# Kernel optimization log

Hardware: AMD Instinct MI355X
Metric: run time of the kernel (lower is better)

Reference implementation:

```python
import jax, jax.numpy as jnp
import numpy as np

NEG_SLOPE = 0.2


def add_self_loops(edge_index, num_nodes):
    loop = jnp.arange(num_nodes, dtype=edge_index.dtype)
    return jnp.concatenate([edge_index, jnp.stack([loop, loop])], axis=1)


def gat_conv(x, edge_index, W, att_src, att_dst, bias, heads, out_ch, concat):
    # x: [N, F_in]; edge_index: [2, E]; W: [F_in, heads*out_ch]
    # att_src/att_dst: [heads, out_ch]; bias: [heads*out_ch] or [out_ch]
    N = x.shape[0]
    ei = add_self_loops(edge_index, N)
    src, dst = ei[0], ei[1]
    xw = (x @ W).reshape(N, heads, out_ch)          # [N, H, C]
    a_src = jnp.einsum('nhc,hc->nh', xw, att_src)    # [N, H]
    a_dst = jnp.einsum('nhc,hc->nh', xw, att_dst)    # [N, H]
    e = a_src[src] + a_dst[dst]                      # [E', H]
    e = jax.nn.leaky_relu(e, NEG_SLOPE)
    # segment softmax over edges grouped by destination node
    e_max = jax.ops.segment_max(e, dst, num_segments=N)  # [N, H]
    e_exp = jnp.exp(e - e_max[dst])
    denom = jax.ops.segment_sum(e_exp, dst, num_segments=N)  # [N, H]
    alpha = e_exp / denom[dst]                       # [E', H]
    msg = xw[src] * alpha[:, :, None]                # [E', H, C]
    out = jax.ops.segment_sum(msg, dst, num_segments=N)  # [N, H, C]
    if concat:
        out = out.reshape(N, heads * out_ch)
    else:
        out = out.mean(axis=1)
    return out + bias


def setup_inputs() -> dict:
    key = jax.random.key(0)
    ks = jax.random.split(key, 10)
    N, E = 100000, 1600000
    F_in, hid, heads, F_out = 128, 32, 4, 40
    s = 0.1
    x = jax.random.normal(ks[0], (N, F_in), dtype=jnp.float32)
    edge_index = jax.random.randint(ks[1], (2, E), 0, N, dtype=jnp.int64)
    W1 = jax.random.normal(ks[2], (F_in, heads * hid), dtype=jnp.float32) * s
    att_src1 = jax.random.normal(ks[3], (heads, hid), dtype=jnp.float32) * s
    att_dst1 = jax.random.normal(ks[4], (heads, hid), dtype=jnp.float32) * s
    b1 = jax.random.normal(ks[5], (heads * hid,), dtype=jnp.float32) * s
    W2 = jax.random.normal(ks[6], (heads * hid, F_out), dtype=jnp.float32) * s
    att_src2 = jax.random.normal(ks[7], (1, F_out), dtype=jnp.float32) * s
    att_dst2 = jax.random.normal(ks[8], (1, F_out), dtype=jnp.float32) * s
    b2 = jax.random.normal(ks[9], (F_out,), dtype=jnp.float32) * s
    return {"x": x, "edge_index": edge_index, "W1": W1, "att_src1": att_src1,
            "att_dst1": att_dst1, "b1": b1, "W2": W2, "att_src2": att_src2,
            "att_dst2": att_dst2, "b2": b2}


def reference(x, edge_index, W1, att_src1, att_dst1, b1, W2, att_src2, att_dst2, b2):
    h = gat_conv(x, edge_index, W1, att_src1, att_dst1, b1, heads=4, out_ch=32, concat=True)
    h = jax.nn.relu(h)
    out = gat_conv(h, edge_index, W2, att_src2, att_dst2, b2, heads=1, out_ch=40, concat=True)
    return out
```

## Files before the change

### kernel.cpp

```cpp
#include <hip/hip_runtime.h>
#include <hip/hip_bf16.h>

#define NEG_SLOPE 0.2f
#define HWREG_XCC_ID_FULL (((32 - 1) << 11) | (0 << 6) | 20)

typedef _Float16 f16;
typedef f16 f16x8 __attribute__((ext_vector_type(8)));
typedef float f32x4 __attribute__((ext_vector_type(4)));

__device__ __forceinline__ float lrelu(float v) { return v > 0.f ? v : NEG_SLOPE * v; }

__device__ __forceinline__ unsigned pack_h2(float a, float b) {
    union { f16 h[2]; unsigned u; } c;
    c.h[0] = (f16)a; c.h[1] = (f16)b;
    return c.u;
}
__device__ __forceinline__ float2 unpack_h2(unsigned u) {
    union { unsigned u; f16 h[2]; } c;
    c.u = u;
    return make_float2((float)c.h[0], (float)c.h[1]);
}

__global__ void k_detect(const int* __restrict__ ei32, int npairs, int* flag) {
    __shared__ int found;
    if (threadIdx.x == 0) found = 0;
    __syncthreads();
    for (int i = threadIdx.x; i < npairs; i += blockDim.x) {
        if (ei32[2 * i + 1] != 0) found = 1;
    }
    __syncthreads();
    if (threadIdx.x == 0) *flag = found ? 0 : 1;
}

__device__ __forceinline__ void load_edge(const void* ei, int f64, int e, int E, int& s, int& d) {
    if (f64) {
        const long long* p = (const long long*)ei;
        s = (int)p[e];
        d = (int)p[(long long)E + e];
    } else {
        const int* p = (const int*)ei;
        s = p[e];
        d = p[E + e];
    }
}

__global__ void k_degree(const void* __restrict__ ei, const int* __restrict__ flag,
                         int* __restrict__ deg_part, int* __restrict__ rank, int N, int E) {
    int e = blockIdx.x * blockDim.x + threadIdx.x;
    if (e >= E) return;
    int s, d;
    load_edge(ei, *flag, e, E, s, d);
    int xcc = (int)(__builtin_amdgcn_s_getreg(HWREG_XCC_ID_FULL) & 7u);
    int lr = atomicAdd(&deg_part[xcc * N + d], 1);
    rank[e] = (xcc << 24) | lr;
}

__global__ void k_sumdeg(int* __restrict__ deg_part, int* __restrict__ deg, int N) {
    int d = blockIdx.x * blockDim.x + threadIdx.x;
    if (d >= N) return;
    int p = 0;
#pragma unroll
    for (int x = 0; x < 8; x++) {
        int t = deg_part[x * N + d];
        deg_part[x * N + d] = p;
        p += t;
    }
    deg[d] = p;
}

__global__ __launch_bounds__(1024) void k_scan_blk(const int* __restrict__ deg,
                                                   int* __restrict__ offsets,
                                                   int* __restrict__ blksum, int N) {
    __shared__ int wsums[16];
    const int t = threadIdx.x;
    const int lane = t & 63;
    const int wid = t >> 6;
    int idx = blockIdx.x * 4096 + t * 4;
    int v0 = (idx + 0 < N) ? deg[idx + 0] : 0;
    int v1 = (idx + 1 < N) ? deg[idx + 1] : 0;
    int v2 = (idx + 2 < N) ? deg[idx + 2] : 0;
    int v3 = (idx + 3 < N) ? deg[idx + 3] : 0;
    int s1 = v0 + v1, s2 = s1 + v2, s3 = s2 + v3;
    int inc = s3;
#pragma unroll
    for (int off = 1; off < 64; off <<= 1) {
        int y = __shfl_up(inc, off);
        if (lane >= off) inc += y;
    }
    if (lane == 63) wsums[wid] = inc;
    __syncthreads();
    if (wid == 0) {
        int v = (lane < 16) ? wsums[lane] : 0;
        int wi = v;
#pragma unroll
        for (int off = 1; off < 16; off <<= 1) {
            int y = __shfl_up(wi, off);
            if (lane >= off) wi += y;
        }
        if (lane < 16) wsums[lane] = wi - v;
        if (lane == 15) blksum[blockIdx.x] = wi;
    }
    __syncthreads();
    int excl = wsums[wid] + (inc - s3);
    if (idx + 0 < N) offsets[idx + 1] = excl + v0;
    if (idx + 1 < N) offsets[idx + 2] = excl + s1;
    if (idx + 2 < N) offsets[idx + 3] = excl + s2;
    if (idx + 3 < N) offsets[idx + 4] = excl + s3;
}

__global__ void k_scan_top(const int* __restrict__ blksum, int* __restrict__ blkoff, int G) {
    int l = threadIdx.x;
    int v = (l < G) ? blksum[l] : 0;
    int inc = v;
#pragma unroll
    for (int off = 1; off < 64; off <<= 1) {
        int y = __shfl_up(inc, off);
        if (l >= off) inc += y;
    }
    if (l < G) blkoff[l] = inc - v;
}

__global__ void k_scan_add(int* __restrict__ offsets, const int* __restrict__ blkoff, int N) {
    int n = blockIdx.x * blockDim.x + threadIdx.x;
    if (n >= N) return;
    offsets[n + 1] += blkoff[n >> 12];
    if (n == 0) offsets[0] = 0;
}

__global__ void k_scatter(const void* __restrict__ ei, const int* __restrict__ flag,
                          const int* __restrict__ offsets, const int* __restrict__ deg_part,
                          const int* __restrict__ rank, int* __restrict__ csr_src,
                          int N, int E) {
    int e = blockIdx.x * blockDim.x + threadIdx.x;
    if (e >= E) return;
    int s, d;
    load_edge(ei, *flag, e, E, s, d);
    int r = rank[e];
    int xcc = r >> 24;
    int lr = r & 0xFFFFFF;
    csr_src[offsets[d] + deg_part[xcc * N + d] + lr] = s;
}

__global__ void k_prep(const float* __restrict__ W1, const float* __restrict__ W2,
                       f16* __restrict__ W1t, f16* __restrict__ W2t) {
    int o = blockIdx.x * 256 + threadIdx.x;
    if (o < 128 * 128) {
        int n = o >> 7, k = o & 127;
        W1t[o] = (f16)W1[k * 128 + n];
    } else {
        int o2 = o - 128 * 128;
        if (o2 < 48 * 128) {
            int n = o2 >> 7, k = o2 & 127;
            W2t[o2] = (f16)(n < 40 ? W2[k * 40 + n] : 0.f);
        }
    }
}

__global__ __launch_bounds__(256) void k_gemm1(const float* __restrict__ X,
                                               const f16* __restrict__ W1t,
                                               f16* __restrict__ Af, int N) {
    __shared__ f16 sA[64 * 136];
    __shared__ f16 sB[128 * 136];
    const int t = threadIdx.x;
    const int row0 = blockIdx.x * 64;

    {
        int r = t >> 2, seg = t & 3;
        int row = row0 + r;
        if (row >= N) row = N - 1;
        const float4* xg = (const float4*)(X + (size_t)row * 128 + seg * 32);
        unsigned tmp[16];
#pragma unroll
        for (int j = 0; j < 8; j++) {
            float4 v = xg[j];
            tmp[2 * j]     = pack_h2(v.x, v.y);
            tmp[2 * j + 1] = pack_h2(v.z, v.w);
        }
        uint4* dst = (uint4*)&sA[r * 136 + seg * 32];
#pragma unroll
        for (int j = 0; j < 4; j++) dst[j] = ((uint4*)tmp)[j];
        int n = t >> 1, half = (t & 1) * 64;
        const uint4* src = (const uint4*)(W1t + n * 128 + half);
        uint4* dw = (uint4*)&sB[n * 136 + half];
#pragma unroll
        for (int j = 0; j < 8; j++) dw[j] = src[j];
    }
    __syncthreads();

    const int w = t >> 6, lane = t & 63, ln = lane & 15, q = lane >> 4;
    f32x4 acc[8];
#pragma unroll
    for (int c = 0; c < 8; c++) acc[c] = (f32x4){0.f, 0.f, 0.f, 0.f};

#pragma unroll
    for (int ks = 0; ks < 4; ks++) {
        f16x8 a = *(const f16x8*)&sA[(w * 16 + ln) * 136 + ks * 32 + q * 8];
#pragma unroll
        for (int c = 0; c < 8; c++) {
            f16x8 b = *(const f16x8*)&sB[(c * 16 + ln) * 136 + ks * 32 + q * 8];
            acc[c] = __builtin_amdgcn_mfma_f32_16x16x32_f16(a, b, acc[c], 0, 0, 0);
        }
    }

#pragma unroll
    for (int c = 0; c < 8; c++)
#pragma unroll
        for (int reg = 0; reg < 4; reg++) {
            int rg = row0 + w * 16 + q * 4 + reg;
            if (rg < N) Af[(size_t)rg * 128 + c * 16 + ln] = (f16)acc[c][reg];
        }
}

__global__ __launch_bounds__(256) void k_gemm2(const f16* __restrict__ Hf,
                                               const f16* __restrict__ W2t,
                                               f16* __restrict__ X2f, int N) {
    __shared__ f16 sA[64 * 136];
    __shared__ f16 sB[48 * 136];
    const int t = threadIdx.x;
    const int row0 = blockIdx.x * 64;
    {
        int r = t >> 2, seg = t & 3;
        int row = row0 + r;
        if (row >= N) row = N - 1;
        const uint4* hg = (const uint4*)(Hf + (size_t)row * 128 + seg * 32);
        uint4* dst = (uint4*)&sA[r * 136 + seg * 32];
#pragma unroll
        for (int j = 0; j < 4; j++) dst[j] = hg[j];
        const uint4* wsrc = (const uint4*)W2t;
#pragma unroll
        for (int u = t; u < 768; u += 256) {
            int o = u * 8;
            int n = o >> 7, ko = o & 127;
            *(uint4*)&sB[n * 136 + ko] = wsrc[u];
        }
    }
    __syncthreads();

    const int w = t >> 6, lane = t & 63, ln = lane & 15, q = lane >> 4;
    f32x4 acc[3];
#pragma unroll
    for (int c = 0; c < 3; c++) acc[c] = (f32x4){0.f, 0.f, 0.f, 0.f};

#pragma unroll
    for (int ks = 0; ks < 4; ks++) {
        f16x8 a = *(const f16x8*)&sA[(w * 16 + ln) * 136 + ks * 32 + q * 8];
#pragma unroll
        for (int c = 0; c < 3; c++) {
            f16x8 b = *(const f16x8*)&sB[(c * 16 + ln) * 136 + ks * 32 + q * 8];
            acc[c] = __builtin_amdgcn_mfma_f32_16x16x32_f16(a, b, acc[c], 0, 0, 0);
        }
    }

#pragma unroll
    for (int c = 0; c < 3; c++) {
        int col = c * 16 + ln;
        if (col < 40) {
#pragma unroll
            for (int reg = 0; reg < 4; reg++) {
                int rg = row0 + w * 16 + q * 4 + reg;
                if (rg < N) X2f[(size_t)rg * 40 + col] = (f16)acc[c][reg];
            }
        }
    }
}

__global__ void k_attn1(const f16* __restrict__ Af, const float* __restrict__ att_s,
                        const float* __restrict__ att_d, float* __restrict__ aS,
                        float* __restrict__ aD, int N) {
    int t = blockIdx.x * blockDim.x + threadIdx.x;
    if (t >= N * 4) return;
    int n = t >> 2, h = t & 3;
    const uint4* xr = (const uint4*)(Af + (size_t)n * 128 + h * 32);
    float ss = 0.f, sd = 0.f;
#pragma unroll
    for (int j = 0; j < 4; j++) {
        uint4 p = xr[j];
        float2 a0 = unpack_h2(p.x), a1 = unpack_h2(p.y), a2 = unpack_h2(p.z), a3 = unpack_h2(p.w);
        float xv[8] = {a0.x, a0.y, a1.x, a1.y, a2.x, a2.y, a3.x, a3.y};
        const float* as_ = att_s + h * 32 + j * 8;
        const float* ad_ = att_d + h * 32 + j * 8;
#pragma unroll
        for (int qq = 0; qq < 8; qq++) {
            ss += xv[qq] * as_[qq];
            sd += xv[qq] * ad_[qq];
        }
    }
    aS[t] = ss;
    aD[t] = sd;
}

__global__ void k_attn2(const f16* __restrict__ X2f, const float* __restrict__ att_s,
                        const float* __restrict__ att_d, float* __restrict__ aS,
                        float* __restrict__ aD, int N) {
    int n = blockIdx.x * blockDim.x + threadIdx.x;
    if (n >= N) return;
    const unsigned* xr = (const unsigned*)(X2f + (size_t)n * 40);
    float ss = 0.f, sd = 0.f;
#pragma unroll
    for (int j = 0; j < 20; j++) {
        float2 v = unpack_h2(xr[j]);
        ss += v.x * att_s[2 * j] + v.y * att_s[2 * j + 1];
        sd += v.x * att_d[2 * j] + v.y * att_d[2 * j + 1];
    }
    aS[n] = ss;
    aD[n] = sd;
}

__global__ __launch_bounds__(256) void k_msg1(const int* __restrict__ offsets,
                                              const int* __restrict__ csr_src,
                                              const float* __restrict__ aS,
                                              const float* __restrict__ aD,
                                              const f16* __restrict__ Af,
                                              const float* __restrict__ b1,
                                              f16* __restrict__ Hf, int N) {
    int n = blockIdx.x * 4 + (threadIdx.x >> 6);
    if (n >= N) return;
    int lane = threadIdx.x & 63;
    int c0 = lane * 2;
    int h = lane >> 4;
    float adh = aD[n * 4 + h];
    float wself = __expf(lrelu(aS[n * 4 + h] + adh));
    float2 pv = unpack_h2(*(const unsigned*)(Af + (size_t)n * 128 + c0));
    float acc0 = wself * pv.x, acc1 = wself * pv.y;
    float wsum = wself;
    int b = offsets[n], e = offsets[n + 1];
    int i = b;
    for (; i + 4 <= e; i += 4) {
        int s0 = csr_src[i], s1 = csr_src[i + 1], s2 = csr_src[i + 2], s3 = csr_src[i + 3];
        unsigned r0 = *(const unsigned*)(Af + (size_t)s0 * 128 + c0);
        unsigned r1 = *(const unsigned*)(Af + (size_t)s1 * 128 + c0);
        unsigned r2 = *(const unsigned*)(Af + (size_t)s2 * 128 + c0);
        unsigned r3 = *(const unsigned*)(Af + (size_t)s3 * 128 + c0);
        float w0 = __expf(lrelu(aS[s0 * 4 + h] + adh));
        float w1 = __expf(lrelu(aS[s1 * 4 + h] + adh));
        float w2 = __expf(lrelu(aS[s2 * 4 + h] + adh));
        float w3 = __expf(lrelu(aS[s3 * 4 + h] + adh));
        float2 f0 = unpack_h2(r0), f1 = unpack_h2(r1), f2 = unpack_h2(r2), f3 = unpack_h2(r3);
        acc0 = fmaf(w0, f0.x, acc0); acc1 = fmaf(w0, f0.y, acc1);
        acc0 = fmaf(w1, f1.x, acc0); acc1 = fmaf(w1, f1.y, acc1);
        acc0 = fmaf(w2, f2.x, acc0); acc1 = fmaf(w2, f2.y, acc1);
        acc0 = fmaf(w3, f3.x, acc0); acc1 = fmaf(w3, f3.y, acc1);
        wsum += (w0 + w1) + (w2 + w3);
    }
    for (; i < e; i++) {
        int s0 = csr_src[i];
        unsigned r0 = *(const unsigned*)(Af + (size_t)s0 * 128 + c0);
        float w0 = __expf(lrelu(aS[s0 * 4 + h] + adh));
        float2 f0 = unpack_h2(r0);
        acc0 = fmaf(w0, f0.x, acc0); acc1 = fmaf(w0, f0.y, acc1);
        wsum += w0;
    }
    float inv = 1.0f / wsum;
    float2 bb = *(const float2*)(b1 + c0);
    *(unsigned*)(Hf + (size_t)n * 128 + c0) =
        pack_h2(fmaxf(fmaf(acc0, inv, bb.x), 0.f), fmaxf(fmaf(acc1, inv, bb.y), 0.f));
}

__global__ __launch_bounds__(256) void k_msg2(const int* __restrict__ offsets,
                                              const int* __restrict__ csr_src,
                                              const float* __restrict__ aS,
                                              const float* __restrict__ aD,
                                              const f16* __restrict__ X2f,
                                              const float* __restrict__ b2,
                                              float* __restrict__ OUT, int N) {
    int wv = threadIdx.x >> 6, lane = threadIdx.x & 63;
    if (lane >= 60) return;
    int g = lane / 20;
    int li = lane - g * 20;
    int n = blockIdx.x * 12 + wv * 3 + g;
    if (n >= N) return;
    int c0 = li * 2;
    float adh = aD[n];
    float wself = __expf(lrelu(aS[n] + adh));
    float2 pv = unpack_h2(*(const unsigned*)(X2f + (size_t)n * 40 + c0));
    float acc0 = wself * pv.x, acc1 = wself * pv.y;
    float wsum = wself;
    int b = offsets[n], e = offsets[n + 1];
    int i = b;
    for (; i + 4 <= e; i += 4) {
        int s0 = csr_src[i], s1 = csr_src[i + 1], s2 = csr_src[i + 2], s3 = csr_src[i + 3];
        unsigned r0 = *(const unsigned*)(X2f + (size_t)s0 * 40 + c0);
        unsigned r1 = *(const unsigned*)(X2f + (size_t)s1 * 40 + c0);
        unsigned r2 = *(const unsigned*)(X2f + (size_t)s2 * 40 + c0);
        unsigned r3 = *(const unsigned*)(X2f + (size_t)s3 * 40 + c0);
        float w0 = __expf(lrelu(aS[s0] + adh));
        float w1 = __expf(lrelu(aS[s1] + adh));
        float w2 = __expf(lrelu(aS[s2] + adh));
        float w3 = __expf(lrelu(aS[s3] + adh));
        float2 f0 = unpack_h2(r0), f1 = unpack_h2(r1), f2 = unpack_h2(r2), f3 = unpack_h2(r3);
        acc0 = fmaf(w0, f0.x, acc0); acc1 = fmaf(w0, f0.y, acc1);
        acc0 = fmaf(w1, f1.x, acc0); acc1 = fmaf(w1, f1.y, acc1);
        acc0 = fmaf(w2, f2.x, acc0); acc1 = fmaf(w2, f2.y, acc1);
        acc0 = fmaf(w3, f3.x, acc0); acc1 = fmaf(w3, f3.y, acc1);
        wsum += (w0 + w1) + (w2 + w3);
    }
    for (; i < e; i++) {
        int s0 = csr_src[i];
        unsigned r0 = *(const unsigned*)(X2f + (size_t)s0 * 40 + c0);
        float w0 = __expf(lrelu(aS[s0] + adh));
        float2 f0 = unpack_h2(r0);
        acc0 = fmaf(w0, f0.x, acc0); acc1 = fmaf(w0, f0.y, acc1);
        wsum += w0;
    }
    float inv = 1.0f / wsum;
    float2 bb = *(const float2*)(b2 + c0);
    *(float2*)(OUT + (size_t)n * 40 + c0) =
        make_float2(fmaf(acc0, inv, bb.x), fmaf(acc1, inv, bb.y));
}

extern "C" void kernel_launch(void* const* d_in, const int* in_sizes, int n_in,
                              void* d_out, int out_size, void* d_ws, size_t ws_size,
                              hipStream_t stream) {
    const float* x   = (const float*)d_in[0];
    const void*  ei  = d_in[1];
    const float* W1  = (const float*)d_in[2];
    const float* as1 = (const float*)d_in[3];
    const float* ad1 = (const float*)d_in[4];
    const float* b1  = (const float*)d_in[5];
    const float* W2  = (const float*)d_in[6];
    const float* as2 = (const float*)d_in[7];
    const float* ad2 = (const float*)d_in[8];
    const float* b2  = (const float*)d_in[9];
    float* out = (float*)d_out;

    const int N = in_sizes[0] / 128;
    const int E = in_sizes[1] / 2;

    char* w = (char*)d_ws;
    auto alloc = [&](size_t bytes) {
        char* p = w;
        w += (bytes + 15) & ~(size_t)15;
        return p;
    };
    int* flag      = (int*)alloc(16);
    int* offsets   = (int*)alloc((size_t)(N + 1) * 4);
    int* deg       = (int*)alloc((size_t)N * 4);
    int* deg_part  = (int*)alloc((size_t)N * 8 * 4);
    int* rank      = (int*)alloc((size_t)E * 4);
    int* csr_src   = (int*)alloc((size_t)E * 4);
    int* blksum    = (int*)alloc(64 * 4);
    int* blkoff    = (int*)alloc(64 * 4);
    float* aS1     = (float*)alloc((size_t)N * 4 * 4);
    float* aD1     = (float*)alloc((size_t)N * 4 * 4);
    float* aS2     = (float*)alloc((size_t)N * 4);
    float* aD2     = (float*)alloc((size_t)N * 4);
    f16* W1t       = (f16*)alloc(128 * 128 * 2);
    f16* W2t       = (f16*)alloc(48 * 128 * 2);
    f16* Af        = (f16*)alloc((size_t)N * 128 * 2);
    f16* X2f       = (f16*)alloc((size_t)N * 40 * 2);
    f16* Hf        = (f16*)alloc((size_t)N * 128 * 2);

    k_detect<<<1, 256, 0, stream>>>((const int*)ei, 1024, flag);
    k_prep<<<88, 256, 0, stream>>>(W1, W2, W1t, W2t);

    hipMemsetAsync(deg_part, 0, (size_t)N * 8 * 4, stream);
    k_degree<<<(E + 255) / 256, 256, 0, stream>>>(ei, flag, deg_part, rank, N, E);
    k_sumdeg<<<(N + 255) / 256, 256, 0, stream>>>(deg_part, deg, N);
    const int G = (N + 4095) / 4096;
    k_scan_blk<<<G, 1024, 0, stream>>>(deg, offsets, blksum, N);
    k_scan_top<<<1, 64, 0, stream>>>(blksum, blkoff, G);
    k_scan_add<<<(N + 255) / 256, 256, 0, stream>>>(offsets, blkoff, N);
    k_scatter<<<(E + 255) / 256, 256, 0, stream>>>(ei, flag, offsets, deg_part, rank,
                                                   csr_src, N, E);

    const int gb = (N + 63) / 64;
    k_gemm1<<<gb, 256, 0, stream>>>(x, W1t, Af, N);
    k_attn1<<<(N * 4 + 255) / 256, 256, 0, stream>>>(Af, as1, ad1, aS1, aD1, N);
    k_msg1<<<(N + 3) / 4, 256, 0, stream>>>(offsets, csr_src, aS1, aD1, Af, b1, Hf, N);

    k_gemm2<<<gb, 256, 0, stream>>>(Hf, W2t, X2f, N);
    k_attn2<<<(N + 255) / 256, 256, 0, stream>>>(X2f, as2, ad2, aS2, aD2, N);
    k_msg2<<<(N + 11) / 12, 256, 0, stream>>>(offsets, csr_src, aS2, aD2, X2f, b2, out, N);
}
```

Before: 396.8 us.

## Restructure GAT aggregation kernels to process multiple edges per wave with wide loads

Rewrites both message-passing kernels so each wave splits into lane groups that handle several incoming edges at once, with each lane loading 16-byte feature chunks instead of 4-byte pairs. Neighbour indices are loaded once per wave and broadcast with ds_bpermute, and partial sums are reduced across groups with shuffles (layer 1) or shared memory (layer 2). Attention scores are pre-scaled by log2(e) so the kernels can use native exp2 and rcp. This aims to raise memory-level parallelism and cut per-edge instruction count in the gather-bound loops, at the cost of idle lanes and extra cross-lane reductions for low-degree nodes.

```diff
diff --git a/kernel.cpp b/kernel.cpp
--- a/kernel.cpp
+++ b/kernel.cpp
@@ -2,6 +2,7 @@
 #include <hip/hip_bf16.h>
 
 #define NEG_SLOPE 0.2f
+#define LOG2E 1.4426950408889634f
 #define HWREG_XCC_ID_FULL (((32 - 1) << 11) | (0 << 6) | 20)
 
 typedef _Float16 f16;
@@ -285,8 +286,8 @@
             sd += xv[qq] * ad_[qq];
         }
     }
-    aS[t] = ss;
-    aD[t] = sd;
+    aS[t] = ss * LOG2E;
+    aD[t] = sd * LOG2E;
 }
 
 __global__ void k_attn2(const f16* __restrict__ X2f, const float* __restrict__ att_s,
@@ -302,8 +303,8 @@
         ss += v.x * att_s[2 * j] + v.y * att_s[2 * j + 1];
         sd += v.x * att_d[2 * j] + v.y * att_d[2 * j + 1];
     }
-    aS[n] = ss;
-    aD[n] = sd;
+    aS[n] = ss * LOG2E;
+    aD[n] = sd * LOG2E;
 }
 
 __global__ __launch_bounds__(256) void k_msg1(const int* __restrict__ offsets,
@@ -313,47 +314,96 @@
                                               const f16* __restrict__ Af,
                                               const float* __restrict__ b1,
                                               f16* __restrict__ Hf, int N) {
-    int n = blockIdx.x * 4 + (threadIdx.x >> 6);
-    if (n >= N) return;
-    int lane = threadIdx.x & 63;
-    int c0 = lane * 2;
-    int h = lane >> 4;
-    float adh = aD[n * 4 + h];
-    float wself = __expf(lrelu(aS[n * 4 + h] + adh));
-    float2 pv = unpack_h2(*(const unsigned*)(Af + (size_t)n * 128 + c0));
-    float acc0 = wself * pv.x, acc1 = wself * pv.y;
-    float wsum = wself;
-    int b = offsets[n], e = offsets[n + 1];
+    const int lane = threadIdx.x & 63;
+    const int n = blockIdx.x * 4 + (threadIdx.x >> 6);
+    const bool node_ok = (n < N);
+    const int g = lane >> 4;
+    const int p = lane & 15;
+    const int h = p >> 2;
+
+    int b = 0, e = 0;
+    float adh = 0.f;
+    if (node_ok) {
+        b = offsets[n];
+        e = offsets[n + 1];
+        adh = aD[n * 4 + h];
+    }
+
+    float acc[8];
+#pragma unroll
+    for (int k = 0; k < 8; k++) acc[k] = 0.f;
+    float wsum = 0.f;
+
+    if (node_ok) {
+        float xs = aS[n * 4 + h] + adh;
+        float ws = __builtin_amdgcn_exp2f(fmaxf(xs, NEG_SLOPE * xs));
+        if (g != 0) ws = 0.f;
+        const f16x8 hv = *(const f16x8*)(Af + (size_t)n * 128 + p * 8);
+#pragma unroll
+        for (int k = 0; k < 8; k++) acc[k] = fmaf(ws, (float)hv[k], acc[k]);
+        wsum = ws;
+    }
+
+    int sreg = 0;
+    if (node_ok && e > b) {
+        int idx = b + lane;
+        if (idx >= e) idx = e - 1;
+        sreg = csr_src[idx];
+    }
+
     int i = b;
-    for (; i + 4 <= e; i += 4) {
-        int s0 = csr_src[i], s1 = csr_src[i + 1], s2 = csr_src[i + 2], s3 = csr_src[i + 3];
-        unsigned r0 = *(const unsigned*)(Af + (size_t)s0 * 128 + c0);
-        unsigned r1 = *(const unsigned*)(Af + (size_t)s1 * 128 + c0);
-        unsigned r2 = *(const unsigned*)(Af + (size_t)s2 * 128 + c0);
-        unsigned r3 = *(const unsigned*)(Af + (size_t)s3 * 128 + c0);
-        float w0 = __expf(lrelu(aS[s0 * 4 + h] + adh));
-        float w1 = __expf(lrelu(aS[s1 * 4 + h] + adh));
-        float w2 = __expf(lrelu(aS[s2 * 4 + h] + adh));
-        float w3 = __expf(lrelu(aS[s3 * 4 + h] + adh));
-        float2 f0 = unpack_h2(r0), f1 = unpack_h2(r1), f2 = unpack_h2(r2), f3 = unpack_h2(r3);
-        acc0 = fmaf(w0, f0.x, acc0); acc1 = fmaf(w0, f0.y, acc1);
-        acc0 = fmaf(w1, f1.x, acc0); acc1 = fmaf(w1, f1.y, acc1);
-        acc0 = fmaf(w2, f2.x, acc0); acc1 = fmaf(w2, f2.y, acc1);
-        acc0 = fmaf(w3, f3.x, acc0); acc1 = fmaf(w3, f3.y, acc1);
-        wsum += (w0 + w1) + (w2 + w3);
-    }
-    for (; i < e; i++) {
-        int s0 = csr_src[i];
-        unsigned r0 = *(const unsigned*)(Af + (size_t)s0 * 128 + c0);
-        float w0 = __expf(lrelu(aS[s0 * 4 + h] + adh));
-        float2 f0 = unpack_h2(r0);
-        acc0 = fmaf(w0, f0.x, acc0); acc1 = fmaf(w0, f0.y, acc1);
-        wsum += w0;
-    }
-    float inv = 1.0f / wsum;
-    float2 bb = *(const float2*)(b1 + c0);
-    *(unsigned*)(Hf + (size_t)n * 128 + c0) =
-        pack_h2(fmaxf(fmaf(acc0, inv, bb.x), 0.f), fmaxf(fmaf(acc1, inv, bb.y), 0.f));
+#pragma unroll 2
+    for (; i < e && (i - b) + 4 <= 64; i += 4) {
+        int j = i + g;
+        bool valid = (j < e);
+        int s = __builtin_amdgcn_ds_bpermute((j - b) << 2, sreg);
+        if (!valid) s = 0;
+        float sv = aS[s * 4 + h];
+        const f16x8 hv = *(const f16x8*)(Af + (size_t)s * 128 + p * 8);
+        float x = sv + adh;
+        float wgt = __builtin_amdgcn_exp2f(fmaxf(x, NEG_SLOPE * x));
+        if (!valid) wgt = 0.f;
+#pragma unroll
+        for (int k = 0; k < 8; k++) acc[k] = fmaf(wgt, (float)hv[k], acc[k]);
+        wsum += wgt;
+    }
+    for (; i < e; i += 4) {
+        int j = i + g;
+        bool valid = (j < e);
+        int jc = valid ? j : (e - 1);
+        int s = csr_src[jc];
+        if (!valid) s = 0;
+        float sv = aS[s * 4 + h];
+        const f16x8 hv = *(const f16x8*)(Af + (size_t)s * 128 + p * 8);
+        float x = sv + adh;
+        float wgt = __builtin_amdgcn_exp2f(fmaxf(x, NEG_SLOPE * x));
+        if (!valid) wgt = 0.f;
+#pragma unroll
+        for (int k = 0; k < 8; k++) acc[k] = fmaf(wgt, (float)hv[k], acc[k]);
+        wsum += wgt;
+    }
+
+#pragma unroll
+    for (int k = 0; k < 8; k++) {
+        acc[k] += __shfl_xor(acc[k], 16);
+        acc[k] += __shfl_xor(acc[k], 32);
+    }
+    wsum += __shfl_xor(wsum, 16);
+    wsum += __shfl_xor(wsum, 32);
+
+    if (node_ok && g == 0) {
+        float inv = __builtin_amdgcn_rcpf(wsum);
+        const float4* bb = (const float4*)(b1 + p * 8);
+        float4 b0 = bb[0], b4 = bb[1];
+        float bv[8] = {b0.x, b0.y, b0.z, b0.w, b4.x, b4.y, b4.z, b4.w};
+        union { f16 h8[8]; uint4 u; } o;
+#pragma unroll
+        for (int k = 0; k < 8; k++) {
+            float v = fmaf(acc[k], inv, bv[k]);
+            o.h8[k] = (f16)fmaxf(v, 0.f);
+        }
+        *(uint4*)(Hf + (size_t)n * 128 + p * 8) = o.u;
+    }
 }
 
 __global__ __launch_bounds__(256) void k_msg2(const int* __restrict__ offsets,
@@ -363,49 +413,94 @@
                                               const f16* __restrict__ X2f,
                                               const float* __restrict__ b2,
                                               float* __restrict__ OUT, int N) {
-    int wv = threadIdx.x >> 6, lane = threadIdx.x & 63;
-    if (lane >= 60) return;
-    int g = lane / 20;
-    int li = lane - g * 20;
-    int n = blockIdx.x * 12 + wv * 3 + g;
-    if (n >= N) return;
-    int c0 = li * 2;
-    float adh = aD[n];
-    float wself = __expf(lrelu(aS[n] + adh));
-    float2 pv = unpack_h2(*(const unsigned*)(X2f + (size_t)n * 40 + c0));
-    float acc0 = wself * pv.x, acc1 = wself * pv.y;
-    float wsum = wself;
-    int b = offsets[n], e = offsets[n + 1];
+    __shared__ float red[4][60][9];
+    const int lane = threadIdx.x & 63;
+    const int wv = threadIdx.x >> 6;
+    const int n = blockIdx.x * 4 + wv;
+    const bool node_ok = (n < N);
+    const int g = lane / 5;
+    const int p = lane % 5;
+    const bool lane_ok = (g < 12);
+
+    int b = 0, e = 0;
+    float adh = 0.f;
+    if (node_ok) {
+        b = offsets[n];
+        e = offsets[n + 1];
+        adh = aD[n];
+    }
+
+    float acc[8];
+#pragma unroll
+    for (int k = 0; k < 8; k++) acc[k] = 0.f;
+    float wsum = 0.f;
+
+    if (node_ok) {
+        float xs = aS[n] + adh;
+        float ws = __builtin_amdgcn_exp2f(fmaxf(xs, NEG_SLOPE * xs));
+        if (!(lane_ok && g == 0)) ws = 0.f;
+        const f16x8 hv = *(const f16x8*)(X2f + (size_t)n * 40 + p * 8);
+#pragma unroll
+        for (int k = 0; k < 8; k++) acc[k] = fmaf(ws, (float)hv[k], acc[k]);
+        wsum = ws;
+    }
+
+    int sreg = 0;
+    if (node_ok && e > b) {
+        int idx = b + lane;
+        if (idx >= e) idx = e - 1;
+        sreg = csr_src[idx];
+    }
+
     int i = b;
-    for (; i + 4 <= e; i += 4) {
-        int s0 = csr_src[i], s1 = csr_src[i + 1], s2 = csr_src[i + 2], s3 = csr_src[i + 3];
-        unsigned r0 = *(const unsigned*)(X2f + (size_t)s0 * 40 + c0);
-        unsigned r1 = *(const unsigned*)(X2f + (size_t)s1 * 40 + c0);
-        unsigned r2 = *(const unsigned*)(X2f + (size_t)s2 * 40 + c0);
-        unsigned r3 = *(const unsigned*)(X2f + (size_t)s3 * 40 + c0);
-        float w0 = __expf(lrelu(aS[s0] + adh));
-        float w1 = __expf(lrelu(aS[s1] + adh));
-        float w2 = __expf(lrelu(aS[s2] + adh));
-        float w3 = __expf(lrelu(aS[s3] + adh));
-        float2 f0 = unpack_h2(r0), f1 = unpack_h2(r1), f2 = unpack_h2(r2), f3 = unpack_h2(r3);
-        acc0 = fmaf(w0, f0.x, acc0); acc1 = fmaf(w0, f0.y, acc1);
-        acc0 = fmaf(w1, f1.x, acc0); acc1 = fmaf(w1, f1.y, acc1);
-        acc0 = fmaf(w2, f2.x, acc0); acc1 = fmaf(w2, f2.y, acc1);
-        acc0 = fmaf(w3, f3.x, acc0); acc1 = fmaf(w3, f3.y, acc1);
-        wsum += (w0 + w1) + (w2 + w3);
-    }
-    for (; i < e; i++) {
-        int s0 = csr_src[i];
-        unsigned r0 = *(const unsigned*)(X2f + (size_t)s0 * 40 + c0);
-        float w0 = __expf(lrelu(aS[s0] + adh));
-        float2 f0 = unpack_h2(r0);
-        acc0 = fmaf(w0, f0.x, acc0); acc1 = fmaf(w0, f0.y, acc1);
-        wsum += w0;
-    }
-    float inv = 1.0f / wsum;
-    float2 bb = *(const float2*)(b2 + c0);
-    *(float2*)(OUT + (size_t)n * 40 + c0) =
-        make_float2(fmaf(acc0, inv, bb.x), fmaf(acc1, inv, bb.y));
+    for (; i < e && (i - b) + 12 <= 64; i += 12) {
+        int j = i + g;
+        bool valid = lane_ok && (j < e);
+        int s = __builtin_amdgcn_ds_bpermute(((j - b) & 63) << 2, sreg);
+        if (!valid) s = 0;
+        float sv = aS[s];
+        const f16x8 hv = *(const f16x8*)(X2f + (size_t)s * 40 + p * 8);
+        float x = sv + adh;
+        float wgt = __builtin_amdgcn_exp2f(fmaxf(x, NEG_SLOPE * x));
+        if (!valid) wgt = 0.f;
+#pragma unroll
+        for (int k = 0; k < 8; k++) acc[k] = fmaf(wgt, (float)hv[k], acc[k]);
+        wsum += wgt;
+    }
+    for (; i < e; i += 12) {
+        int j = i + g;
+        bool valid = lane_ok && (j < e);
+        int jc = (j < e) ? j : (e - 1);
+        int s = csr_src[jc];
+        if (!valid) s = 0;
+        float sv = aS[s];
+        const f16x8 hv = *(const f16x8*)(X2f + (size_t)s * 40 + p * 8);
+        float x = sv + adh;
+        float wgt = __builtin_amdgcn_exp2f(fmaxf(x, NEG_SLOPE * x));
+        if (!valid) wgt = 0.f;
+#pragma unroll
+        for (int k = 0; k < 8; k++) acc[k] = fmaf(wgt, (float)hv[k], acc[k]);
+        wsum += wgt;
+    }
+
+    if (lane_ok) {
+#pragma unroll
+        for (int k = 0; k < 8; k++) red[wv][lane][k] = acc[k];
+        red[wv][lane][8] = wsum;
+    }
+    __syncthreads();
+
+    if (node_ok && lane < 40) {
+        int pp = lane >> 3, kk = lane & 7;
+        float s_ = 0.f, ws_ = 0.f;
+#pragma unroll
+        for (int gg = 0; gg < 12; gg++) {
+            s_  += red[wv][gg * 5 + pp][kk];
+            ws_ += red[wv][gg * 5][8];
+        }
+        float inv = __builtin_amdgcn_rcpf(ws_);
+        OUT[(size_t)n * 40 + lane] = fmaf(s_, inv, b2[lane]);
+    }
 }
 
 extern "C" void kernel_launch(void* const* d_in, const int* in_sizes, int n_in,
@@ -470,5 +565,5 @@
 
     k_gemm2<<<gb, 256, 0, stream>>>(Hf, W2t, X2f, N);
     k_attn2<<<(N + 255) / 256, 256, 0, stream>>>(X2f, as2, ad2, aS2, aD2, N);
-    k_msg2<<<(N + 11) / 12, 256, 0, stream>>>(offsets, csr_src, aS2, aD2, X2f, b2, out, N);
-}
+    k_msg2<<<(N + 3) / 4, 256, 0, stream>>>(offsets, csr_src, aS2, aD2, X2f, b2, out, N);
+}
```

New measurement: 390.8 us. Within noise of the previous version (-1.5%).
